# Kernel tuning notes

Hardware: AMD Instinct MI355X
Metric: run time of the kernel (lower is better)

The kernel has to match this reference:

```python
import jax, jax.numpy as jnp
import numpy as np


def setup_inputs() -> dict:
    key = jax.random.key(0)
    ks = jax.random.split(key, 6)
    B, T, D, N = 8, 4096, 1024, 16
    s = 0.02  # small init scale for linear weights
    return {
        "x": jax.random.normal(ks[0], (B, T, D), jnp.float32),
        "Wd": jax.random.normal(ks[1], (D, D), jnp.float32) * s,
        "bd": jnp.zeros((D,), jnp.float32),
        "Wb": jax.random.normal(ks[2], (D, N), jnp.float32) * s,
        "bb": jnp.zeros((N,), jnp.float32),
        "Wc": jax.random.normal(ks[3], (D, N), jnp.float32) * s,
        "bc": jnp.zeros((N,), jnp.float32),
        "Wo": jax.random.normal(ks[4], (D, D), jnp.float32) * s,
        "bo": jnp.zeros((D,), jnp.float32),
        "A": jax.random.normal(ks[5], (D, N), jnp.float32) * 0.01,
    }


def reference(x, Wd, bd, Wb, bb, Wc, bc, Wo, bo, A):
    # x: (B, T, D). All per-step projections are time-independent -> batch them.
    delta = jax.nn.softplus(x @ Wd + bd)              # (B, T, D)
    dbar = jnp.mean(delta, axis=-1, keepdims=True)    # (B, T, 1) scalar gate per step
    Bt = x @ Wb + bb                                  # (B, T, N)
    Ct = x @ Wc + bc                                  # (B, T, N)
    sA = jax.nn.sigmoid(jnp.mean(A, axis=0))          # (N,)

    a = 1.0 - dbar                                    # (B, T, 1) decay
    b = dbar * Bt * sA                                # (B, T, N) input injection

    def step(h, ab):
        at, bt = ab                                   # at: (B,1), bt: (B,N)
        h = h * at + bt
        return h, h

    h0 = jnp.zeros((x.shape[0], A.shape[1]), x.dtype)
    # scan over time axis (leading)
    _, hs = jax.lax.scan(step, h0, (jnp.swapaxes(a, 0, 1), jnp.swapaxes(b, 0, 1)))
    hs = jnp.swapaxes(hs, 0, 1)                       # (B, T, N)

    y = jnp.sum(hs * Ct, axis=-1, keepdims=True) * x  # (B, T, D); (h*C).sum expanded * x
    return y @ Wo + bo
```

## Files before the change

kernel.cpp:

```cpp
#include <hip/hip_runtime.h>
#include <hip/hip_bf16.h>


typedef __bf16 bfx4 __attribute__((ext_vector_type(4)));
typedef __bf16 bfx8 __attribute__((ext_vector_type(8)));
typedef float  f32x4 __attribute__((ext_vector_type(4)));

#define M_ROWS 32768
#define DDIM   1024
#define NSTATE 16
#define TLEN   4096
#define BATCH  8
#define CHUNK  32
#define NCHUNK 128
#define NGROUP (BATCH * NCHUNK)

#define BK     32
#define KT     (DDIM / BK)
#define TILEE  16384

__global__ __launch_bounds__(256) void transpose_w_kernel(
    const float* __restrict__ Wd, const float* __restrict__ Wo,
    __bf16* __restrict__ WdT, __bf16* __restrict__ WoT)
{
    __shared__ float tile[32][33];
    const int bid = blockIdx.x;
    const float* src = (bid < 1024) ? Wd : Wo;
    __bf16* dst = (bid < 1024) ? WdT : WoT;
    const int t = bid & 1023;
    const int tr = t >> 5, tc = t & 31;
    const int tx = threadIdx.x & 31, ty = threadIdx.x >> 5;
#pragma unroll
    for (int i = 0; i < 4; ++i) {
        int r = ty + i * 8;
        tile[r][tx] = src[(size_t)(tr * 32 + r) * 1024 + tc * 32 + tx];
    }
    __syncthreads();
#pragma unroll
    for (int i = 0; i < 4; ++i) {
        int r = ty + i * 8;
        dst[(size_t)(tc * 32 + r) * 1024 + tr * 32 + tx] = (__bf16)tile[tx][r];
    }
}

__global__ __launch_bounds__(256) void wbc_kernel(
    const float* __restrict__ Wb, const float* __restrict__ Wc,
    __bf16* __restrict__ Wbc)
{
    int idx = blockIdx.x * 256 + threadIdx.x;
    int n2 = idx >> 10, k = idx & 1023;
    float v = (n2 < 16) ? Wb[k * 16 + n2] : Wc[k * 16 + (n2 - 16)];
    Wbc[idx] = (__bf16)v;
}

__global__ __launch_bounds__(256) void sA_kernel(const float* __restrict__ A,
                                                 float* __restrict__ sA)
{
    __shared__ float red[256];
    int tid = threadIdx.x;
    int n = tid & 15, part = tid >> 4;
    float sum = 0.f;
    for (int k = part * 64; k < part * 64 + 64; ++k) sum += A[k * 16 + n];
    red[tid] = sum;
    __syncthreads();
    if (tid < 16) {
        float tot = 0.f;
        for (int p = 0; p < 16; ++p) tot += red[p * 16 + tid];
        sA[tid] = 1.f / (1.f + expf(-tot * (1.f / 1024.f)));
    }
}

__global__ __launch_bounds__(256) void cast_kernel(const float* __restrict__ x,
                                                   __bf16* __restrict__ xb)
{
    size_t i = ((size_t)blockIdx.x * 256 + threadIdx.x) * 8;
    const float4* xg = (const float4*)(x + i);
    float4 v0 = xg[0], v1 = xg[1];
    bfx8 o;
    o[0] = (__bf16)v0.x; o[1] = (__bf16)v0.y; o[2] = (__bf16)v0.z; o[3] = (__bf16)v0.w;
    o[4] = (__bf16)v1.x; o[5] = (__bf16)v1.y; o[6] = (__bf16)v1.z; o[7] = (__bf16)v1.w;
    *(bfx8*)(xb + i) = o;
}

__global__ __launch_bounds__(256) void btct_kernel(
    const __bf16* __restrict__ xb, const __bf16* __restrict__ Wbc,
    const float* __restrict__ bb, const float* __restrict__ bc,
    float* __restrict__ Bt, float* __restrict__ Ct)
{
    const int wid = blockIdx.x * 4 + (threadIdx.x >> 6);
    const int lane = threadIdx.x & 63;
    const int quad = lane >> 4, l15 = lane & 15;
    const int mbase = wid * 16;
    const __bf16* ga = xb + (size_t)(mbase + l15) * 1024 + quad * 8;
    const __bf16* gb = Wbc + (size_t)l15 * 1024 + quad * 8;
    const __bf16* gc = Wbc + (size_t)(16 + l15) * 1024 + quad * 8;
    f32x4 accB = {0.f, 0.f, 0.f, 0.f};
    f32x4 accC = {0.f, 0.f, 0.f, 0.f};
#pragma unroll 4
    for (int k = 0; k < 1024; k += 32) {
        bfx8 a = *(const bfx8*)ga;  ga += 32;
        bfx8 b = *(const bfx8*)gb;  gb += 32;
        bfx8 c = *(const bfx8*)gc;  gc += 32;
        accB = __builtin_amdgcn_mfma_f32_16x16x32_bf16(a, b, accB, 0, 0, 0);
        accC = __builtin_amdgcn_mfma_f32_16x16x32_bf16(a, c, accC, 0, 0, 0);
    }
#pragma unroll
    for (int r = 0; r < 4; ++r) {
        int row = mbase + quad * 4 + r;
        Bt[row * 16 + l15] = accB[r] + bb[l15];
        Ct[row * 16 + l15] = accC[r] + bc[l15];
    }
}

__device__ __forceinline__ void gload16(const void* g, void* l)
{
    __builtin_amdgcn_global_load_lds((__attribute__((address_space(1))) void*)g,
                                     (__attribute__((address_space(3))) void*)l,
                                     16, 0, 0);
}

__device__ __forceinline__ void tile_swizzle256(int L, int& mtile, int& ntile)
{
    int xcd = L & 7;
    int s = L >> 3;
    mtile = xcd * 16 + (s >> 2);
    ntile = s & 3;
}

__device__ __forceinline__ void stage_tile(const __bf16* pA0, const __bf16* pA1,
                                           const __bf16* pB0, const __bf16* pB1,
                                           __bf16* lbase, int tid, int t)
{
    const size_t ko = (size_t)t * BK;
    __bf16* ba = lbase;
    __bf16* bb2 = lbase + 8192;
    gload16(pA0 + ko, ba + tid * 8);
    gload16(pA1 + ko, ba + 4096 + tid * 8);
    gload16(pB0 + ko, bb2 + tid * 8);
    gload16(pB1 + ko, bb2 + 4096 + tid * 8);
}

__device__ __forceinline__ void compute_tile(const __bf16* lbase,
                                             int aoff, int boff,
                                             f32x4 acc[8][4])
{
    const __bf16* Al = lbase;
    const __bf16* Bl = lbase + 8192;
    bfx8 bfr[4];
#pragma unroll
    for (int j = 0; j < 4; ++j)
        bfr[j] = *(const bfx8*)(Bl + boff + j * 512);
    bfx8 af[8];
#pragma unroll
    for (int i = 0; i < 8; ++i)
        af[i] = *(const bfx8*)(Al + aoff + i * 512);
    __builtin_amdgcn_s_setprio(1);
#pragma unroll
    for (int i = 0; i < 8; ++i)
#pragma unroll
        for (int j = 0; j < 4; ++j)
            acc[i][j] = __builtin_amdgcn_mfma_f32_16x16x32_bf16(
                af[i], bfr[j], acc[i][j], 0, 0, 0);
    __builtin_amdgcn_s_setprio(0);
}

__device__ __forceinline__ void gemm_core256(const __bf16* __restrict__ Abuf,
                                             const __bf16* __restrict__ Bbuf,
                                             __bf16* lds,
                                             int mbase, int nbase,
                                             f32x4 acc[8][4])
{
    const int tid = threadIdx.x;
    const int lane = tid & 63;
    const int w = tid >> 6;
    const int quad = lane >> 4, l15 = lane & 15;
    const int wm = w >> 2, wn = w & 3;

    const int row0 = ((tid >> 6) << 4) + ((tid >> 2) & 15);
    const int kc   = (tid & 3) ^ ((tid >> 3) & 3);
    const __bf16* pA0 = Abuf + (size_t)(mbase + row0) * DDIM + kc * 8;
    const __bf16* pA1 = pA0 + (size_t)128 * DDIM;
    const __bf16* pB0 = Bbuf + (size_t)(nbase + row0) * DDIM + kc * 8;
    const __bf16* pB1 = pB0 + (size_t)128 * DDIM;

    const int vsw  = l15 * 4 + (quad ^ ((l15 >> 1) & 3));
    const int aoff = wm * 8 * 512 + vsw * 8;
    const int boff = wn * 4 * 512 + vsw * 8;

    stage_tile(pA0, pA1, pB0, pB1, lds + 0 * TILEE, tid, 0);
    stage_tile(pA0, pA1, pB0, pB1, lds + 1 * TILEE, tid, 1);
    stage_tile(pA0, pA1, pB0, pB1, lds + 2 * TILEE, tid, 2);

#pragma unroll 1
    for (int t = 0; t < KT - 2; ++t) {
        asm volatile("s_waitcnt vmcnt(8)" ::: "memory");
        __builtin_amdgcn_s_barrier();
        __builtin_amdgcn_sched_barrier(0);
        if (t < KT - 3)
            stage_tile(pA0, pA1, pB0, pB1, lds + ((t + 3) & 3) * TILEE, tid, t + 3);
        compute_tile(lds + (t & 3) * TILEE, aoff, boff, acc);
    }
    asm volatile("s_waitcnt vmcnt(4)" ::: "memory");
    __builtin_amdgcn_s_barrier();
    __builtin_amdgcn_sched_barrier(0);
    compute_tile(lds + ((KT - 2) & 3) * TILEE, aoff, boff, acc);
    asm volatile("s_waitcnt vmcnt(0)" ::: "memory");
    __builtin_amdgcn_s_barrier();
    __builtin_amdgcn_sched_barrier(0);
    compute_tile(lds + ((KT - 1) & 3) * TILEE, aoff, boff, acc);
}

__global__ __launch_bounds__(512, 2) void gemm1_kernel(
    const __bf16* __restrict__ xb, const __bf16* __restrict__ WdT,
    const float* __restrict__ bd, float* __restrict__ dbar)
{
    __shared__ __bf16 lds[4 * TILEE];
    f32x4 acc[8][4];
    f32x4 z4 = {0.f, 0.f, 0.f, 0.f};
#pragma unroll
    for (int i = 0; i < 8; ++i)
#pragma unroll
        for (int j = 0; j < 4; ++j) acc[i][j] = z4;

    int mtile, ntile;
    tile_swizzle256(blockIdx.x, mtile, ntile);
    const int mbase = mtile * 256;
    const int nbase = ntile * 256;
    gemm_core256(xb, WdT, lds, mbase, nbase, acc);

    const int lane = threadIdx.x & 63;
    const int w = threadIdx.x >> 6;
    const int quad = lane >> 4, l15 = lane & 15;
    const int wm = w >> 2, wn = w & 3;
    const float invD = 1.0f / 1024.0f;
#pragma unroll
    for (int i = 0; i < 8; ++i) {
#pragma unroll
        for (int r = 0; r < 4; ++r) {
            float sp = 0.f;
#pragma unroll
            for (int j = 0; j < 4; ++j) {
                int col = nbase + wn * 64 + j * 16 + l15;
                float z = acc[i][j][r] + bd[col];
                sp += fmaxf(z, 0.f) + __logf(1.f + __expf(-fabsf(z)));
            }
#pragma unroll
            for (int off = 1; off < 16; off <<= 1) sp += __shfl_xor(sp, off, 16);
            if (l15 == 0) {
                int row = mbase + wm * 128 + i * 16 + quad * 4 + r;
                atomicAdd(&dbar[row], sp * invD);
            }
        }
    }
}

__global__ __launch_bounds__(512, 2) void gemm2_kernel(
    const __bf16* __restrict__ xb, const __bf16* __restrict__ WoT,
    const float* __restrict__ srow, const float* __restrict__ bo,
    float* __restrict__ out)
{
    __shared__ __bf16 lds[4 * TILEE];
    f32x4 acc[8][4];
    f32x4 z4 = {0.f, 0.f, 0.f, 0.f};
#pragma unroll
    for (int i = 0; i < 8; ++i)
#pragma unroll
        for (int j = 0; j < 4; ++j) acc[i][j] = z4;

    int mtile, ntile;
    tile_swizzle256(blockIdx.x, mtile, ntile);
    const int mbase = mtile * 256;
    const int nbase = ntile * 256;
    gemm_core256(xb, WoT, lds, mbase, nbase, acc);

    const int lane = threadIdx.x & 63;
    const int w = threadIdx.x >> 6;
    const int quad = lane >> 4, l15 = lane & 15;
    const int wm = w >> 2, wn = w & 3;
#pragma unroll
    for (int i = 0; i < 8; ++i) {
        int row0 = mbase + wm * 128 + i * 16 + quad * 4;
#pragma unroll
        for (int r = 0; r < 4; ++r) {
            float sv = srow[row0 + r];
#pragma unroll
            for (int j = 0; j < 4; ++j) {
                int col = nbase + wn * 64 + j * 16 + l15;
                out[(size_t)(row0 + r) * 1024 + col] = sv * acc[i][j][r] + bo[col];
            }
        }
    }
}

__global__ __launch_bounds__(256) void scan_kernel(
    const float* __restrict__ dbar, const float* __restrict__ Bt,
    const float* __restrict__ Ct, const float* __restrict__ sA,
    float* __restrict__ s_local, float* __restrict__ pbuf,
    float* __restrict__ Pc, float* __restrict__ Hend)
{
    int tid = threadIdx.x;
    int gid = blockIdx.x * 16 + (tid >> 4);
    int n = tid & 15;
    int b = gid >> 7;
    int c = gid & 127;
    float sAn = sA[n];
    float h = 0.f, p = 1.f;
    int row = b * TLEN + c * CHUNK;
#pragma unroll 4
    for (int t = 0; t < CHUNK; ++t, ++row) {
        float d = dbar[row];
        float btv = Bt[row * 16 + n];
        float ctv = Ct[row * 16 + n];
        float a = 1.f - d;
        h = h * a + d * sAn * btv;
        p *= a;
        float prod = h * ctv;
#pragma unroll
        for (int off = 1; off < 16; off <<= 1) prod += __shfl_xor(prod, off, 16);
        if (n == 0) { s_local[row] = prod; pbuf[row] = p; }
    }
    Hend[gid * 16 + n] = h;
    if (n == 0) Pc[gid] = p;
}

__global__ __launch_bounds__(128) void stitch_kernel(
    const float* __restrict__ Pc, const float* __restrict__ Hend,
    float* __restrict__ h0buf)
{
    int tid = threadIdx.x;
    int b = tid >> 4, n = tid & 15;
    float h0 = 0.f;
#pragma unroll 8
    for (int c = 0; c < NCHUNK; ++c) {
        int g = b * NCHUNK + c;
        h0buf[g * 16 + n] = h0;
        h0 = Pc[g] * h0 + Hend[g * 16 + n];
    }
}

__global__ __launch_bounds__(256) void fixup_kernel(
    const float* __restrict__ s_local, const float* __restrict__ pbuf,
    const float* __restrict__ h0buf, const float* __restrict__ Ct,
    float* __restrict__ sbuf)
{
    int row = blockIdx.x * 256 + threadIdx.x;
    int b = row >> 12, t = row & 4095;
    int g = b * NCHUNK + (t / CHUNK);
    const float4* h4 = (const float4*)(h0buf + g * 16);
    const float4* c4 = (const float4*)(Ct + (size_t)row * 16);
    float dot = 0.f;
#pragma unroll
    for (int q = 0; q < 4; ++q) {
        float4 hv = h4[q], cv = c4[q];
        dot += hv.x * cv.x + hv.y * cv.y + hv.z * cv.z + hv.w * cv.w;
    }
    sbuf[row] = s_local[row] + pbuf[row] * dot;
}

extern "C" void kernel_launch(void* const* d_in, const int* in_sizes, int n_in,
                              void* d_out, int out_size, void* d_ws, size_t ws_size,
                              hipStream_t stream)
{
    const float* x  = (const float*)d_in[0];
    const float* Wd = (const float*)d_in[1];
    const float* bd = (const float*)d_in[2];
    const float* Wb = (const float*)d_in[3];
    const float* bb = (const float*)d_in[4];
    const float* Wc = (const float*)d_in[5];
    const float* bc = (const float*)d_in[6];
    const float* Wo = (const float*)d_in[7];
    const float* bo = (const float*)d_in[8];
    const float* A  = (const float*)d_in[9];
    float* out = (float*)d_out;

    char* base = (char*)d_ws;
    size_t off = 0;
    auto alloc = [&](size_t bytes) -> void* {
        void* p = base + off;
        off = (off + bytes + 255) & ~(size_t)255;
        return p;
    };
    __bf16* xb   = (__bf16*)alloc((size_t)M_ROWS * DDIM * 2);
    __bf16* WdT  = (__bf16*)alloc((size_t)DDIM * DDIM * 2);
    __bf16* WoT  = (__bf16*)alloc((size_t)DDIM * DDIM * 2);
    __bf16* Wbc  = (__bf16*)alloc(32 * 1024 * 2);
    float* sAbuf = (float*)alloc(64);
    float* dbar  = (float*)alloc(M_ROWS * 4);
    float* Bt    = (float*)alloc((size_t)M_ROWS * 16 * 4);
    float* Ct    = (float*)alloc((size_t)M_ROWS * 16 * 4);
    float* s_loc = (float*)alloc(M_ROWS * 4);
    float* pbuf  = (float*)alloc(M_ROWS * 4);
    float* sbuf  = (float*)alloc(M_ROWS * 4);
    float* Pc    = (float*)alloc(NGROUP * 4);
    float* Hend  = (float*)alloc(NGROUP * 16 * 4);
    float* h0buf = (float*)alloc(NGROUP * 16 * 4);

    transpose_w_kernel<<<2048, 256, 0, stream>>>(Wd, Wo, WdT, WoT);
    wbc_kernel<<<128, 256, 0, stream>>>(Wb, Wc, Wbc);
    sA_kernel<<<1, 256, 0, stream>>>(A, sAbuf);
    cast_kernel<<<M_ROWS * DDIM / 8 / 256, 256, 0, stream>>>(x, xb);
    (void)hipMemsetAsync(dbar, 0, M_ROWS * 4, stream);
    btct_kernel<<<512, 256, 0, stream>>>(xb, Wbc, bb, bc, Bt, Ct);
    gemm1_kernel<<<512, 512, 0, stream>>>(xb, WdT, bd, dbar);
    scan_kernel<<<NGROUP / 16, 256, 0, stream>>>(dbar, Bt, Ct, sAbuf, s_loc, pbuf, Pc, Hend);
    stitch_kernel<<<1, 128, 0, stream>>>(Pc, Hend, h0buf);
    fixup_kernel<<<M_ROWS / 256, 256, 0, stream>>>(s_loc, pbuf, h0buf, Ct, sbuf);
    gemm2_kernel<<<512, 512, 0, stream>>>(xb, WoT, sbuf, bo, out);
}
```

Before: 459.2 us.

## Fuse scan/stitch/fixup into one kernel and split GEMM k-step into halves

Two unrelated changes. First, the three-kernel chunked scan (scan, stitch, fixup) becomes a single kernel with one block per batch. It does a two-pass chunked scan of 16 chunks of 256 steps, stitches the chunk states in shared memory, then recomputes with the correct initial state. Second, the GEMM main loop is restructured so each k-step issues half the LDS fragment loads and half the global prefetches between two MFMA halves, with an extra barrier. The scan now launches only 8 blocks, which leaves most CUs idle and makes each thread run a serial 512-step chain. That could be slower than the old 1024-group version even though it saves launches and intermediate traffic.

```diff
diff --git a/kernel.cpp b/kernel.cpp
--- a/kernel.cpp
+++ b/kernel.cpp
@@ -11,9 +11,6 @@
 #define NSTATE 16
 #define TLEN   4096
 #define BATCH  8
-#define CHUNK  32
-#define NCHUNK 128
-#define NGROUP (BATCH * NCHUNK)
 
 #define BK     32
 #define KT     (DDIM / BK)
@@ -140,30 +137,6 @@
     gload16(pB1 + ko, bb2 + 4096 + tid * 8);
 }
 
-__device__ __forceinline__ void compute_tile(const __bf16* lbase,
-                                             int aoff, int boff,
-                                             f32x4 acc[8][4])
-{
-    const __bf16* Al = lbase;
-    const __bf16* Bl = lbase + 8192;
-    bfx8 bfr[4];
-#pragma unroll
-    for (int j = 0; j < 4; ++j)
-        bfr[j] = *(const bfx8*)(Bl + boff + j * 512);
-    bfx8 af[8];
-#pragma unroll
-    for (int i = 0; i < 8; ++i)
-        af[i] = *(const bfx8*)(Al + aoff + i * 512);
-    __builtin_amdgcn_s_setprio(1);
-#pragma unroll
-    for (int i = 0; i < 8; ++i)
-#pragma unroll
-        for (int j = 0; j < 4; ++j)
-            acc[i][j] = __builtin_amdgcn_mfma_f32_16x16x32_bf16(
-                af[i], bfr[j], acc[i][j], 0, 0, 0);
-    __builtin_amdgcn_s_setprio(0);
-}
-
 __device__ __forceinline__ void gemm_core256(const __bf16* __restrict__ Abuf,
                                              const __bf16* __restrict__ Bbuf,
                                              __bf16* lds,
@@ -192,22 +165,56 @@
     stage_tile(pA0, pA1, pB0, pB1, lds + 2 * TILEE, tid, 2);
 
 #pragma unroll 1
-    for (int t = 0; t < KT - 2; ++t) {
-        asm volatile("s_waitcnt vmcnt(8)" ::: "memory");
+    for (int t = 0; t < KT; ++t) {
+        if (t < KT - 2)       asm volatile("s_waitcnt vmcnt(8)" ::: "memory");
+        else if (t == KT - 2) asm volatile("s_waitcnt vmcnt(4)" ::: "memory");
+        else                  asm volatile("s_waitcnt vmcnt(0)" ::: "memory");
         __builtin_amdgcn_s_barrier();
         __builtin_amdgcn_sched_barrier(0);
-        if (t < KT - 3)
-            stage_tile(pA0, pA1, pB0, pB1, lds + ((t + 3) & 3) * TILEE, tid, t + 3);
-        compute_tile(lds + (t & 3) * TILEE, aoff, boff, acc);
-    }
-    asm volatile("s_waitcnt vmcnt(4)" ::: "memory");
-    __builtin_amdgcn_s_barrier();
-    __builtin_amdgcn_sched_barrier(0);
-    compute_tile(lds + ((KT - 2) & 3) * TILEE, aoff, boff, acc);
-    asm volatile("s_waitcnt vmcnt(0)" ::: "memory");
-    __builtin_amdgcn_s_barrier();
-    __builtin_amdgcn_sched_barrier(0);
-    compute_tile(lds + ((KT - 1) & 3) * TILEE, aoff, boff, acc);
+
+        const __bf16* Al = lds + (t & 3) * TILEE;
+        const __bf16* Bl = Al + 8192;
+        const size_t ko3 = (size_t)(t + 3) * BK;
+        __bf16* lb3 = lds + ((t + 3) & 3) * TILEE;
+
+        bfx8 bfr[4], af[4];
+#pragma unroll
+        for (int j = 0; j < 4; ++j) bfr[j] = *(const bfx8*)(Bl + boff + j * 512);
+#pragma unroll
+        for (int i = 0; i < 4; ++i) af[i]  = *(const bfx8*)(Al + aoff + i * 512);
+        if (t < KT - 3) {
+            gload16(pA0 + ko3, lb3 + tid * 8);
+            gload16(pA1 + ko3, lb3 + 4096 + tid * 8);
+        }
+        asm volatile("s_waitcnt lgkmcnt(0)" ::: "memory");
+        __builtin_amdgcn_sched_barrier(0);
+        __builtin_amdgcn_s_setprio(1);
+#pragma unroll
+        for (int i = 0; i < 4; ++i)
+#pragma unroll
+            for (int j = 0; j < 4; ++j)
+                acc[i][j] = __builtin_amdgcn_mfma_f32_16x16x32_bf16(
+                    af[i], bfr[j], acc[i][j], 0, 0, 0);
+        __builtin_amdgcn_s_setprio(0);
+        __builtin_amdgcn_s_barrier();
+
+#pragma unroll
+        for (int i = 0; i < 4; ++i) af[i] = *(const bfx8*)(Al + aoff + (4 + i) * 512);
+        if (t < KT - 3) {
+            gload16(pB0 + ko3, lb3 + 8192 + tid * 8);
+            gload16(pB1 + ko3, lb3 + 8192 + 4096 + tid * 8);
+        }
+        asm volatile("s_waitcnt lgkmcnt(0)" ::: "memory");
+        __builtin_amdgcn_sched_barrier(0);
+        __builtin_amdgcn_s_setprio(1);
+#pragma unroll
+        for (int i = 0; i < 4; ++i)
+#pragma unroll
+            for (int j = 0; j < 4; ++j)
+                acc[4 + i][j] = __builtin_amdgcn_mfma_f32_16x16x32_bf16(
+                    af[i], bfr[j], acc[4 + i][j], 0, 0, 0);
+        __builtin_amdgcn_s_setprio(0);
+    }
 }
 
 __global__ __launch_bounds__(512, 2) void gemm1_kernel(
@@ -292,69 +299,56 @@
     }
 }
 
-__global__ __launch_bounds__(256) void scan_kernel(
+__global__ __launch_bounds__(256) void scan_fused_kernel(
     const float* __restrict__ dbar, const float* __restrict__ Bt,
     const float* __restrict__ Ct, const float* __restrict__ sA,
-    float* __restrict__ s_local, float* __restrict__ pbuf,
-    float* __restrict__ Pc, float* __restrict__ Hend)
-{
-    int tid = threadIdx.x;
-    int gid = blockIdx.x * 16 + (tid >> 4);
-    int n = tid & 15;
-    int b = gid >> 7;
-    int c = gid & 127;
-    float sAn = sA[n];
+    float* __restrict__ sbuf)
+{
+    __shared__ float Hend_s[16][16];
+    __shared__ float P_s[16];
+    __shared__ float H0_s[16][16];
+    const int tid = threadIdx.x;
+    const int g = tid >> 4, n = tid & 15;
+    const int b = blockIdx.x;
+    const float sAn = sA[n];
+    const int row0 = b * TLEN + g * 256;
+
     float h = 0.f, p = 1.f;
-    int row = b * TLEN + c * CHUNK;
 #pragma unroll 4
-    for (int t = 0; t < CHUNK; ++t, ++row) {
+    for (int t = 0; t < 256; ++t) {
+        int row = row0 + t;
+        float d = dbar[row];
+        float btv = Bt[row * 16 + n];
+        float a = 1.f - d;
+        h = h * a + d * sAn * btv;
+        p *= a;
+    }
+    Hend_s[g][n] = h;
+    if (n == 0) P_s[g] = p;
+    __syncthreads();
+    if (tid < 16) {
+        float h0 = 0.f;
+#pragma unroll
+        for (int c = 0; c < 16; ++c) {
+            H0_s[c][tid] = h0;
+            h0 = P_s[c] * h0 + Hend_s[c][tid];
+        }
+    }
+    __syncthreads();
+    h = H0_s[g][n];
+#pragma unroll 4
+    for (int t = 0; t < 256; ++t) {
+        int row = row0 + t;
         float d = dbar[row];
         float btv = Bt[row * 16 + n];
         float ctv = Ct[row * 16 + n];
         float a = 1.f - d;
         h = h * a + d * sAn * btv;
-        p *= a;
         float prod = h * ctv;
 #pragma unroll
         for (int off = 1; off < 16; off <<= 1) prod += __shfl_xor(prod, off, 16);
-        if (n == 0) { s_local[row] = prod; pbuf[row] = p; }
-    }
-    Hend[gid * 16 + n] = h;
-    if (n == 0) Pc[gid] = p;
-}
-
-__global__ __launch_bounds__(128) void stitch_kernel(
-    const float* __restrict__ Pc, const float* __restrict__ Hend,
-    float* __restrict__ h0buf)
-{
-    int tid = threadIdx.x;
-    int b = tid >> 4, n = tid & 15;
-    float h0 = 0.f;
-#pragma unroll 8
-    for (int c = 0; c < NCHUNK; ++c) {
-        int g = b * NCHUNK + c;
-        h0buf[g * 16 + n] = h0;
-        h0 = Pc[g] * h0 + Hend[g * 16 + n];
-    }
-}
-
-__global__ __launch_bounds__(256) void fixup_kernel(
-    const float* __restrict__ s_local, const float* __restrict__ pbuf,
-    const float* __restrict__ h0buf, const float* __restrict__ Ct,
-    float* __restrict__ sbuf)
-{
-    int row = blockIdx.x * 256 + threadIdx.x;
-    int b = row >> 12, t = row & 4095;
-    int g = b * NCHUNK + (t / CHUNK);
-    const float4* h4 = (const float4*)(h0buf + g * 16);
-    const float4* c4 = (const float4*)(Ct + (size_t)row * 16);
-    float dot = 0.f;
-#pragma unroll
-    for (int q = 0; q < 4; ++q) {
-        float4 hv = h4[q], cv = c4[q];
-        dot += hv.x * cv.x + hv.y * cv.y + hv.z * cv.z + hv.w * cv.w;
-    }
-    sbuf[row] = s_local[row] + pbuf[row] * dot;
+        if (n == 0) sbuf[row] = prod;
+    }
 }
 
 extern "C" void kernel_launch(void* const* d_in, const int* in_sizes, int n_in,
@@ -388,12 +382,7 @@
     float* dbar  = (float*)alloc(M_ROWS * 4);
     float* Bt    = (float*)alloc((size_t)M_ROWS * 16 * 4);
     float* Ct    = (float*)alloc((size_t)M_ROWS * 16 * 4);
-    float* s_loc = (float*)alloc(M_ROWS * 4);
-    float* pbuf  = (float*)alloc(M_ROWS * 4);
     float* sbuf  = (float*)alloc(M_ROWS * 4);
-    float* Pc    = (float*)alloc(NGROUP * 4);
-    float* Hend  = (float*)alloc(NGROUP * 16 * 4);
-    float* h0buf = (float*)alloc(NGROUP * 16 * 4);
 
     transpose_w_kernel<<<2048, 256, 0, stream>>>(Wd, Wo, WdT, WoT);
     wbc_kernel<<<128, 256, 0, stream>>>(Wb, Wc, Wbc);
@@ -402,8 +391,6 @@
     (void)hipMemsetAsync(dbar, 0, M_ROWS * 4, stream);
     btct_kernel<<<512, 256, 0, stream>>>(xb, Wbc, bb, bc, Bt, Ct);
     gemm1_kernel<<<512, 512, 0, stream>>>(xb, WdT, bd, dbar);
-    scan_kernel<<<NGROUP / 16, 256, 0, stream>>>(dbar, Bt, Ct, sAbuf, s_loc, pbuf, Pc, Hend);
-    stitch_kernel<<<1, 128, 0, stream>>>(Pc, Hend, h0buf);
-    fixup_kernel<<<M_ROWS / 256, 256, 0, stream>>>(s_loc, pbuf, h0buf, Ct, sbuf);
+    scan_fused_kernel<<<BATCH, 256, 0, stream>>>(dbar, Bt, Ct, sAbuf, sbuf);
     gemm2_kernel<<<512, 512, 0, stream>>>(xb, WoT, sbuf, bo, out);
 }
```

After: 547.3 us. 1.19x slower.
